# Kernel optimization log

Hardware: AMD Instinct MI355X
Metric: run time of the kernel (lower is better)

## Reference

```python
import jax, jax.numpy as jnp
import numpy as np
from jax import lax


def setup_inputs() -> dict:
    key = jax.random.key(0)
    k1, k2 = jax.random.split(key)
    x = jax.random.normal(k1, (32, 128, 64, 64), dtype=jnp.float32)
    # learned kernel, original shape (k, k, in_channels, out_channels)
    K = jax.random.normal(k2, (3, 3, 128, 256), dtype=jnp.float32) * 0.05
    return {"x": x, "K": K}


def reference(x, K):
    stride, padding = 1, 1
    kh = K.shape[0]
    C = K.shape[2]
    O = K.shape[3]
    H = x.shape[-1]
    P = H + 2 * padding
    out_size = (P - kh) // stride + 1
    # Original pairs x-patches flattened as (C, kh, kw) with K flattened
    # row-major as (kh, kw, C), matched purely by flat index. Equivalent to a
    # standard conv with the weight buffer reinterpreted as (C, kh, kw, O):
    W = K.reshape(-1, O).reshape(C, kh, kh, O).transpose(3, 0, 1, 2)  # (O,C,kh,kw)
    out = lax.conv_general_dilated(
        x, W,
        window_strides=(stride, stride),
        padding=[(padding, padding), (padding, padding)],
        dimension_numbers=("NCHW", "OIHW", "NCHW"),
    )  # (B, O, out_size, out_size)
    # Original loop uses range(0, P - kh, stride) (missing +1): when
    # (P - kh) % stride == 0 the last output row/col is never written (stays 0).
    n_filled = -(-(P - kh) // stride)  # ceil((P-kh)/stride), static
    if n_filled < out_size:
        out = out.at[:, :, n_filled:, :].set(0.0)
        out = out.at[:, :, :, n_filled:].set(0.0)
    return out
```

## Files before the change

### kernel.cpp

```cpp
#include <hip/hip_runtime.h>
#include <hip/hip_bf16.h>

typedef __attribute__((ext_vector_type(8))) short bf16x8;
typedef __attribute__((ext_vector_type(4))) float f32x4;

#define CIN   128
#define HW    64
#define OUTC  256

#define BP_OFF     33554432ULL
#define ZP_OFF     34144256ULL
#define WS_NEEDED  34148352ULL

#define SB  __builtin_amdgcn_s_barrier()
#define SCB __builtin_amdgcn_sched_barrier(0)
#define WAITV(N) asm volatile("s_waitcnt vmcnt(" #N ")" ::: "memory")
#define WAITL    asm volatile("s_waitcnt lgkmcnt(0)" ::: "memory")
#define MFMA(a, b, c) __builtin_amdgcn_mfma_f32_16x16x32_bf16(a, b, c, 0, 0, 0)

#define MFMA16(MB, A0, A1, A2, A3, B0, B1, B2, B3) do {            \
    __builtin_amdgcn_s_setprio(1);                                 \
    acc[MB+0][0] = MFMA(A0, B0, acc[MB+0][0]);                     \
    acc[MB+1][0] = MFMA(A1, B0, acc[MB+1][0]);                     \
    acc[MB+2][0] = MFMA(A2, B0, acc[MB+2][0]);                     \
    acc[MB+3][0] = MFMA(A3, B0, acc[MB+3][0]);                     \
    acc[MB+0][1] = MFMA(A0, B1, acc[MB+0][1]);                     \
    acc[MB+1][1] = MFMA(A1, B1, acc[MB+1][1]);                     \
    acc[MB+2][1] = MFMA(A2, B1, acc[MB+2][1]);                     \
    acc[MB+3][1] = MFMA(A3, B1, acc[MB+3][1]);                     \
    acc[MB+0][2] = MFMA(A0, B2, acc[MB+0][2]);                     \
    acc[MB+1][2] = MFMA(A1, B2, acc[MB+1][2]);                     \
    acc[MB+2][2] = MFMA(A2, B2, acc[MB+2][2]);                     \
    acc[MB+3][2] = MFMA(A3, B2, acc[MB+3][2]);                     \
    acc[MB+0][3] = MFMA(A0, B3, acc[MB+0][3]);                     \
    acc[MB+1][3] = MFMA(A1, B3, acc[MB+1][3]);                     \
    acc[MB+2][3] = MFMA(A2, B3, acc[MB+2][3]);                     \
    acc[MB+3][3] = MFMA(A3, B3, acc[MB+3][3]);                     \
    __builtin_amdgcn_s_setprio(0);                                 \
} while (0)

__global__ __launch_bounds__(256) void conv_prep(const float* __restrict__ X,
                                                 const float* __restrict__ Kw,
                                                 __hip_bfloat16* __restrict__ Xt,
                                                 __hip_bfloat16* __restrict__ Bp,
                                                 __hip_bfloat16* __restrict__ zp) {
    const int blk = blockIdx.x;
    if (blk < 2048) {
        __shared__ __hip_bfloat16 L[64][136];
        const int b = blk >> 6;
        const int y = blk & 63;
        const int x = threadIdx.x & 63;
        const int c0 = (threadIdx.x >> 6) * 32;
        const float* src = X + (((long)(b * CIN + c0) * HW + y) * HW + x);
        #pragma unroll
        for (int j = 0; j < 32; j += 2) {
            float v0 = src[(long)j * (HW * HW)];
            float v1 = src[(long)(j + 1) * (HW * HW)];
            __hip_bfloat162 p;
            p.x = __float2bfloat16(v0);
            p.y = __float2bfloat16(v1);
            *reinterpret_cast<__hip_bfloat162*>(&L[x][c0 + j]) = p;
        }
        __syncthreads();
        __hip_bfloat16* dst = Xt + (long)blk * (64 * 128);
        #pragma unroll
        for (int it = 0; it < 4; ++it) {
            int G = it * 256 + threadIdx.x;
            int xx = G >> 4, g = G & 15;
            bf16x8 v = *reinterpret_cast<const bf16x8*>(&L[xx][g * 8]);
            *reinterpret_cast<bf16x8*>(&dst[(long)G * 8]) = v;
        }
    } else if (blk < 2112) {
        for (int idx = (blk - 2048) * 256 + threadIdx.x; idx < 294912; idx += 64 * 256) {
            int c  = idx & 127;
            int n  = (idx >> 7) & 255;
            int ij = idx >> 15;
            Bp[idx] = __float2bfloat16(Kw[((c * 9 + ij) << 8) + n]);
        }
    } else {
        *reinterpret_cast<float4*>((char*)zp + threadIdx.x * 16) = float4{0.f, 0.f, 0.f, 0.f};
    }
}

__global__ __launch_bounds__(512, 2) void conv_igemm5(
    const __hip_bfloat16* __restrict__ Xt,
    const __hip_bfloat16* __restrict__ Bp,
    const __hip_bfloat16* __restrict__ zp,
    float* __restrict__ out)
{
    __shared__ __hip_bfloat16 As[2][2][256 * 32];
    __shared__ __hip_bfloat16 Bs[2][2][256 * 32];

    const int tid  = threadIdx.x;
    const int wv   = tid >> 6;
    const int lane = tid & 63;
    const int l16  = lane & 15;
    const int d16  = lane >> 4;
    const int wr   = wv >> 2;
    const int wc   = wv & 3;

    const int bid   = blockIdx.x;
    const int mtile = (bid & 7) * 64 + (bid >> 3);
    const int b  = mtile >> 4;
    const int y0 = (mtile & 15) * 4;

    const int srow = lane >> 2;
    const int sg   = lane & 3;

    f32x4 acc[8][4] = {};

    const int r0  = wv * 32 + srow;
    const int r1  = r0 + 16;
    const int G0  = (sg - (r0 >> 1)) & 3;
    const int G1  = (sg - (r1 >> 1)) & 3;
    const int xr0 = r0 & 63, xr1 = r1 & 63;
    const int yy0 = y0 + (r0 >> 6), yy1 = y0 + (r1 >> 6);
    const __hip_bfloat16* pA0 = Xt + (((long)b * 4096 + yy0 * 64 + xr0) * 128 + G0 * 8);
    const __hip_bfloat16* pA1 = Xt + (((long)b * 4096 + yy1 * 64 + xr1) * 128 + G1 * 8);
    const __hip_bfloat16* pB0 = Bp + ((long)r0 * 128 + G0 * 8);
    const __hip_bfloat16* pB1 = Bp + ((long)r1 * 128 + G1 * 8);
    const int ldsOff0 = (wv * 32) * 32;
    const int ldsOff1 = (wv * 32 + 16) * 32;

    auto stageA = [&](int t, int kh) {
        const int ij = t >> 1;
        const int c0 = (t & 1) * 64 + kh * 32;
        const int di = ij / 3 - 1;
        const int dj = ij % 3 - 1;
        const long off = (long)(di * 64 + dj) * 128 + c0;
        const bool ok0 = ((unsigned)(xr0 + dj) < 64u) && ((unsigned)(yy0 + di) < 64u);
        const bool ok1 = ((unsigned)(xr1 + dj) < 64u) && ((unsigned)(yy1 + di) < 64u);
        const __hip_bfloat16* g0 = ok0 ? pA0 + off : zp + c0;
        const __hip_bfloat16* g1 = ok1 ? pA1 + off : zp + c0;
        __builtin_amdgcn_global_load_lds(
            (const __attribute__((address_space(1))) void*)g0,
            (__attribute__((address_space(3))) void*)(&As[t & 1][kh][0] + ldsOff0), 16, 0, 0);
        __builtin_amdgcn_global_load_lds(
            (const __attribute__((address_space(1))) void*)g1,
            (__attribute__((address_space(3))) void*)(&As[t & 1][kh][0] + ldsOff1), 16, 0, 0);
    };
    auto stageB = [&](int t, int kh) {
        const long off = (long)(t >> 1) * 32768 + (t & 1) * 64 + kh * 32;
        __builtin_amdgcn_global_load_lds(
            (const __attribute__((address_space(1))) void*)(pB0 + off),
            (__attribute__((address_space(3))) void*)(&Bs[t & 1][kh][0] + ldsOff0), 16, 0, 0);
        __builtin_amdgcn_global_load_lds(
            (const __attribute__((address_space(1))) void*)(pB1 + off),
            (__attribute__((address_space(3))) void*)(&Bs[t & 1][kh][0] + ldsOff1), 16, 0, 0);
    };
    auto rdA = [&](int d, int kh, int mi) -> bf16x8 {
        const int m = wr * 128 + mi * 16 + l16;
        const int s = (d16 + (m >> 1)) & 3;
        return *reinterpret_cast<const bf16x8*>(&As[d][kh][m * 32 + s * 8]);
    };
    auto rdB = [&](int d, int kh, int ni) -> bf16x8 {
        const int n = wc * 64 + ni * 16 + l16;
        const int s = (d16 + (n >> 1)) & 3;
        return *reinterpret_cast<const bf16x8*>(&Bs[d][kh][n * 32 + s * 8]);
    };

    stageA(0, 0); stageB(0, 0);
    stageA(0, 1); stageB(0, 1);
    stageA(1, 0); stageB(1, 0);

    #define PAIR(D, KH, VW, STA, STB)                                        \
    do {                                                                     \
        STA;                                                                 \
        VW; SB; SCB;                                                         \
        bf16x8 A0 = rdA(D, KH, 0), A1 = rdA(D, KH, 1),                       \
               A2 = rdA(D, KH, 2), A3 = rdA(D, KH, 3);                       \
        bf16x8 B0 = rdB(D, KH, 0), B1 = rdB(D, KH, 1),                       \
               B2 = rdB(D, KH, 2), B3 = rdB(D, KH, 3);                       \
        WAITL; SCB;                                                          \
        MFMA16(0, A0, A1, A2, A3, B0, B1, B2, B3);                           \
        SB;                                                                  \
        STB;                                                                 \
        bf16x8 A4 = rdA(D, KH, 4), A5 = rdA(D, KH, 5),                       \
               A6 = rdA(D, KH, 6), A7 = rdA(D, KH, 7);                       \
        SB; WAITL; SCB;                                                      \
        MFMA16(4, A4, A5, A6, A7, B0, B1, B2, B3);                           \
        SB;                                                                  \
    } while (0)

    #pragma unroll
    for (int i = 0; i < 8; ++i) {
        const int t = 2 * i;
        PAIR(0, 0, WAITV(10), stageA(t + 1, 1), stageB(t + 1, 1));
        PAIR(0, 1, WAITV(10), stageA(t + 2, 0), stageB(t + 2, 0));
        PAIR(1, 0, WAITV(10), stageA(t + 2, 1), stageB(t + 2, 1));
        PAIR(1, 1, WAITV(10), stageA(t + 3, 0), stageB(t + 3, 0));
    }
    PAIR(0, 0, WAITV(10), stageA(17, 1), stageB(17, 1));
    PAIR(0, 1, WAITV(8),  (void)0, (void)0);
    PAIR(1, 0, WAITV(4),  (void)0, (void)0);
    PAIR(1, 1, WAITV(0),  (void)0, (void)0);
    #undef PAIR

    #pragma unroll
    for (int mi = 0; mi < 8; ++mi) {
        const int m  = wr * 128 + mi * 16 + d16 * 4;
        const int x0 = m & 63;
        const int y  = y0 + (m >> 6);
        #pragma unroll
        for (int ni = 0; ni < 4; ++ni) {
            const int o = wc * 64 + ni * 16 + l16;
            float4 v;
            v.x = acc[mi][ni][0];
            v.y = acc[mi][ni][1];
            v.z = acc[mi][ni][2];
            v.w = acc[mi][ni][3];
            if (y == HW - 1) { v.x = v.y = v.z = v.w = 0.f; }
            if (x0 + 3 == HW - 1) v.w = 0.f;
            *reinterpret_cast<float4*>(
                out + ((long)(b * OUTC + o) * 4096 + y * 64 + x0)) = v;
        }
    }
}

__global__ __launch_bounds__(256) void conv_igemm_bf16(
    const float* __restrict__ X, const float* __restrict__ Kw, float* __restrict__ out) {
    __shared__ __hip_bfloat16 As[128][40];
    __shared__ __hip_bfloat16 Bs[128][40];
    const int tid = threadIdx.x, wave = tid >> 6, lane = tid & 63;
    const int l16 = lane & 15, d16 = lane >> 4;
    const int m_base = blockIdx.x * 128;
    const int b = m_base >> 12, y0 = (m_base & 4095) >> 6;
    const int n_base = blockIdx.y * 128;
    const int wm = (wave >> 1) * 64, wn = (wave & 1) * 64;
    f32x4 acc[4][4] = {};
    const int smm = tid & 127, ccb = tid >> 7;
    const int sx = smm & 63, syr = smm >> 6;
    for (int ij = 0; ij < 9; ++ij) {
        const int di = ij / 3 - 1, dj = ij % 3 - 1;
        const int xp = sx + dj, yp = y0 + syr + di;
        const bool ok = ((unsigned)xp < 64u) && ((unsigned)yp < 64u);
        const long xbase = (((long)b * CIN) * HW + yp) * HW + xp;
        for (int c0 = 0; c0 < CIN; c0 += 32) {
            for (int cc = ccb; cc < 32; cc += 2) {
                float v = ok ? X[xbase + (long)(c0 + cc) * 4096] : 0.f;
                As[smm][cc] = __float2bfloat16(v);
                Bs[smm][cc] = __float2bfloat16(Kw[((c0 + cc) * 9 + ij) * OUTC + n_base + smm]);
            }
            __syncthreads();
            bf16x8 afrag[4], bfrag[4];
            for (int mi = 0; mi < 4; ++mi)
                afrag[mi] = *reinterpret_cast<const bf16x8*>(&As[wm + mi * 16 + l16][d16 * 8]);
            for (int ni = 0; ni < 4; ++ni)
                bfrag[ni] = *reinterpret_cast<const bf16x8*>(&Bs[wn + ni * 16 + l16][d16 * 8]);
            for (int mi = 0; mi < 4; ++mi)
                for (int ni = 0; ni < 4; ++ni)
                    acc[mi][ni] = __builtin_amdgcn_mfma_f32_16x16x32_bf16(
                        afrag[mi], bfrag[ni], acc[mi][ni], 0, 0, 0);
            __syncthreads();
        }
    }
    for (int mi = 0; mi < 4; ++mi)
        for (int ni = 0; ni < 4; ++ni)
            for (int r = 0; r < 4; ++r) {
                const int mm = wm + mi * 16 + d16 * 4 + r;
                const int nn = wn + ni * 16 + l16;
                const int y = y0 + (mm >> 6), x = mm & 63, o = n_base + nn;
                float v = acc[mi][ni][r];
                if (y == 63 || x == 63) v = 0.f;
                out[(((long)b * OUTC + o) * HW + y) * HW + x] = v;
            }
}

extern "C" void kernel_launch(void* const* d_in, const int* in_sizes, int n_in,
                              void* d_out, int out_size, void* d_ws, size_t ws_size,
                              hipStream_t stream) {
    const float* X  = (const float*)d_in[0];
    const float* Kw = (const float*)d_in[1];
    float* out = (float*)d_out;

    if (ws_size >= WS_NEEDED) {
        char* ws = (char*)d_ws;
        __hip_bfloat16* Xt = (__hip_bfloat16*)ws;
        __hip_bfloat16* Bp = (__hip_bfloat16*)(ws + BP_OFF);
        __hip_bfloat16* zp = (__hip_bfloat16*)(ws + ZP_OFF);
        conv_prep<<<dim3(2113), dim3(256), 0, stream>>>(X, Kw, Xt, Bp, zp);
        conv_igemm5<<<dim3(512), dim3(512), 0, stream>>>(Xt, Bp, zp, out);
    } else {
        conv_igemm_bf16<<<dim3(1024, 2), dim3(256), 0, stream>>>(X, Kw, out);
    }
}
```

Measured before the change: 107.4 us.

## Restructure conv main loop into 4-stage LDS ring with one barrier pair per k-step

Replaces the hand-interleaved double-buffer PAIR schedule, which split each 32-wide k-slice into two half-MFMA batches with mid-step staging, with a uniform 4-deep ring buffer of 32-channel slices. Each of the 36 iterations reads all A/B fragments into registers, issues the global-to-LDS load for slice H+3, waits on vmcnt, then runs all 32 MFMAs under raised priority. This simplifies the schedule and keeps three slices in flight. In exchange it holds 12 fragment vectors live at once, which raises register pressure, and the compiler has less fine-grained interleaving of LDS reads with MFMAs.

```diff
diff --git a/kernel.cpp b/kernel.cpp
--- a/kernel.cpp
+++ b/kernel.cpp
@@ -15,29 +15,7 @@
 #define SB  __builtin_amdgcn_s_barrier()
 #define SCB __builtin_amdgcn_sched_barrier(0)
 #define WAITV(N) asm volatile("s_waitcnt vmcnt(" #N ")" ::: "memory")
-#define WAITL    asm volatile("s_waitcnt lgkmcnt(0)" ::: "memory")
 #define MFMA(a, b, c) __builtin_amdgcn_mfma_f32_16x16x32_bf16(a, b, c, 0, 0, 0)
-
-#define MFMA16(MB, A0, A1, A2, A3, B0, B1, B2, B3) do {            \
-    __builtin_amdgcn_s_setprio(1);                                 \
-    acc[MB+0][0] = MFMA(A0, B0, acc[MB+0][0]);                     \
-    acc[MB+1][0] = MFMA(A1, B0, acc[MB+1][0]);                     \
-    acc[MB+2][0] = MFMA(A2, B0, acc[MB+2][0]);                     \
-    acc[MB+3][0] = MFMA(A3, B0, acc[MB+3][0]);                     \
-    acc[MB+0][1] = MFMA(A0, B1, acc[MB+0][1]);                     \
-    acc[MB+1][1] = MFMA(A1, B1, acc[MB+1][1]);                     \
-    acc[MB+2][1] = MFMA(A2, B1, acc[MB+2][1]);                     \
-    acc[MB+3][1] = MFMA(A3, B1, acc[MB+3][1]);                     \
-    acc[MB+0][2] = MFMA(A0, B2, acc[MB+0][2]);                     \
-    acc[MB+1][2] = MFMA(A1, B2, acc[MB+1][2]);                     \
-    acc[MB+2][2] = MFMA(A2, B2, acc[MB+2][2]);                     \
-    acc[MB+3][2] = MFMA(A3, B2, acc[MB+3][2]);                     \
-    acc[MB+0][3] = MFMA(A0, B3, acc[MB+0][3]);                     \
-    acc[MB+1][3] = MFMA(A1, B3, acc[MB+1][3]);                     \
-    acc[MB+2][3] = MFMA(A2, B3, acc[MB+2][3]);                     \
-    acc[MB+3][3] = MFMA(A3, B3, acc[MB+3][3]);                     \
-    __builtin_amdgcn_s_setprio(0);                                 \
-} while (0)
 
 __global__ __launch_bounds__(256) void conv_prep(const float* __restrict__ X,
                                                  const float* __restrict__ Kw,
@@ -82,14 +60,14 @@
     }
 }
 
-__global__ __launch_bounds__(512, 2) void conv_igemm5(
+__global__ __launch_bounds__(512, 2) void conv_igemm6(
     const __hip_bfloat16* __restrict__ Xt,
     const __hip_bfloat16* __restrict__ Bp,
     const __hip_bfloat16* __restrict__ zp,
     float* __restrict__ out)
 {
-    __shared__ __hip_bfloat16 As[2][2][256 * 32];
-    __shared__ __hip_bfloat16 Bs[2][2][256 * 32];
+    __shared__ __hip_bfloat16 As[4][256 * 32];
+    __shared__ __hip_bfloat16 Bs[4][256 * 32];
 
     const int tid  = threadIdx.x;
     const int wv   = tid >> 6;
@@ -122,79 +100,67 @@
     const int ldsOff0 = (wv * 32) * 32;
     const int ldsOff1 = (wv * 32 + 16) * 32;
 
-    auto stageA = [&](int t, int kh) {
-        const int ij = t >> 1;
-        const int c0 = (t & 1) * 64 + kh * 32;
+    auto stage = [&](int S) {
+        const int ij = S >> 2;
+        const int c0 = (S & 3) * 32;
         const int di = ij / 3 - 1;
         const int dj = ij % 3 - 1;
-        const long off = (long)(di * 64 + dj) * 128 + c0;
+        const long offA = (long)(di * 64 + dj) * 128 + c0;
         const bool ok0 = ((unsigned)(xr0 + dj) < 64u) && ((unsigned)(yy0 + di) < 64u);
         const bool ok1 = ((unsigned)(xr1 + dj) < 64u) && ((unsigned)(yy1 + di) < 64u);
-        const __hip_bfloat16* g0 = ok0 ? pA0 + off : zp + c0;
-        const __hip_bfloat16* g1 = ok1 ? pA1 + off : zp + c0;
-        __builtin_amdgcn_global_load_lds(
-            (const __attribute__((address_space(1))) void*)g0,
-            (__attribute__((address_space(3))) void*)(&As[t & 1][kh][0] + ldsOff0), 16, 0, 0);
-        __builtin_amdgcn_global_load_lds(
-            (const __attribute__((address_space(1))) void*)g1,
-            (__attribute__((address_space(3))) void*)(&As[t & 1][kh][0] + ldsOff1), 16, 0, 0);
+        const __hip_bfloat16* gA0 = ok0 ? pA0 + offA : zp + c0;
+        const __hip_bfloat16* gA1 = ok1 ? pA1 + offA : zp + c0;
+        __hip_bfloat16* ldsA = &As[S & 3][0];
+        __builtin_amdgcn_global_load_lds(
+            (const __attribute__((address_space(1))) void*)gA0,
+            (__attribute__((address_space(3))) void*)(ldsA + ldsOff0), 16, 0, 0);
+        __builtin_amdgcn_global_load_lds(
+            (const __attribute__((address_space(1))) void*)gA1,
+            (__attribute__((address_space(3))) void*)(ldsA + ldsOff1), 16, 0, 0);
+        const long offB = (long)ij * 32768 + c0;
+        __hip_bfloat16* ldsB = &Bs[S & 3][0];
+        __builtin_amdgcn_global_load_lds(
+            (const __attribute__((address_space(1))) void*)(pB0 + offB),
+            (__attribute__((address_space(3))) void*)(ldsB + ldsOff0), 16, 0, 0);
+        __builtin_amdgcn_global_load_lds(
+            (const __attribute__((address_space(1))) void*)(pB1 + offB),
+            (__attribute__((address_space(3))) void*)(ldsB + ldsOff1), 16, 0, 0);
     };
-    auto stageB = [&](int t, int kh) {
-        const long off = (long)(t >> 1) * 32768 + (t & 1) * 64 + kh * 32;
-        __builtin_amdgcn_global_load_lds(
-            (const __attribute__((address_space(1))) void*)(pB0 + off),
-            (__attribute__((address_space(3))) void*)(&Bs[t & 1][kh][0] + ldsOff0), 16, 0, 0);
-        __builtin_amdgcn_global_load_lds(
-            (const __attribute__((address_space(1))) void*)(pB1 + off),
-            (__attribute__((address_space(3))) void*)(&Bs[t & 1][kh][0] + ldsOff1), 16, 0, 0);
-    };
-    auto rdA = [&](int d, int kh, int mi) -> bf16x8 {
-        const int m = wr * 128 + mi * 16 + l16;
-        const int s = (d16 + (m >> 1)) & 3;
-        return *reinterpret_cast<const bf16x8*>(&As[d][kh][m * 32 + s * 8]);
-    };
-    auto rdB = [&](int d, int kh, int ni) -> bf16x8 {
-        const int n = wc * 64 + ni * 16 + l16;
-        const int s = (d16 + (n >> 1)) & 3;
-        return *reinterpret_cast<const bf16x8*>(&Bs[d][kh][n * 32 + s * 8]);
-    };
-
-    stageA(0, 0); stageB(0, 0);
-    stageA(0, 1); stageB(0, 1);
-    stageA(1, 0); stageB(1, 0);
-
-    #define PAIR(D, KH, VW, STA, STB)                                        \
-    do {                                                                     \
-        STA;                                                                 \
-        VW; SB; SCB;                                                         \
-        bf16x8 A0 = rdA(D, KH, 0), A1 = rdA(D, KH, 1),                       \
-               A2 = rdA(D, KH, 2), A3 = rdA(D, KH, 3);                       \
-        bf16x8 B0 = rdB(D, KH, 0), B1 = rdB(D, KH, 1),                       \
-               B2 = rdB(D, KH, 2), B3 = rdB(D, KH, 3);                       \
-        WAITL; SCB;                                                          \
-        MFMA16(0, A0, A1, A2, A3, B0, B1, B2, B3);                           \
-        SB;                                                                  \
-        STB;                                                                 \
-        bf16x8 A4 = rdA(D, KH, 4), A5 = rdA(D, KH, 5),                       \
-               A6 = rdA(D, KH, 6), A7 = rdA(D, KH, 7);                       \
-        SB; WAITL; SCB;                                                      \
-        MFMA16(4, A4, A5, A6, A7, B0, B1, B2, B3);                           \
-        SB;                                                                  \
-    } while (0)
+
+    stage(0); stage(1); stage(2);
+    WAITV(8);
+    SCB; SB;
 
     #pragma unroll
-    for (int i = 0; i < 8; ++i) {
-        const int t = 2 * i;
-        PAIR(0, 0, WAITV(10), stageA(t + 1, 1), stageB(t + 1, 1));
-        PAIR(0, 1, WAITV(10), stageA(t + 2, 0), stageB(t + 2, 0));
-        PAIR(1, 0, WAITV(10), stageA(t + 2, 1), stageB(t + 2, 1));
-        PAIR(1, 1, WAITV(10), stageA(t + 3, 0), stageB(t + 3, 0));
-    }
-    PAIR(0, 0, WAITV(10), stageA(17, 1), stageB(17, 1));
-    PAIR(0, 1, WAITV(8),  (void)0, (void)0);
-    PAIR(1, 0, WAITV(4),  (void)0, (void)0);
-    PAIR(1, 1, WAITV(0),  (void)0, (void)0);
-    #undef PAIR
+    for (int H = 0; H < 36; ++H) {
+        const int RB = H & 3;
+        bf16x8 Af[8], Bf[4];
+        #pragma unroll
+        for (int mi = 0; mi < 8; ++mi) {
+            const int m = wr * 128 + mi * 16 + l16;
+            const int s = (d16 + (m >> 1)) & 3;
+            Af[mi] = *reinterpret_cast<const bf16x8*>(&As[RB][m * 32 + s * 8]);
+        }
+        #pragma unroll
+        for (int ni = 0; ni < 4; ++ni) {
+            const int n = wc * 64 + ni * 16 + l16;
+            const int s = (d16 + (n >> 1)) & 3;
+            Bf[ni] = *reinterpret_cast<const bf16x8*>(&Bs[RB][n * 32 + s * 8]);
+        }
+        if (H < 33) stage(H + 3);
+        if (H < 33)       WAITV(8);
+        else if (H == 33) WAITV(4);
+        else if (H == 34) WAITV(0);
+        SCB; SB;
+        __builtin_amdgcn_s_setprio(1);
+        #pragma unroll
+        for (int ni = 0; ni < 4; ++ni)
+            #pragma unroll
+            for (int mi = 0; mi < 8; ++mi)
+                acc[mi][ni] = MFMA(Af[mi], Bf[ni], acc[mi][ni]);
+        __builtin_amdgcn_s_setprio(0);
+        SCB; SB;
+    }
 
     #pragma unroll
     for (int mi = 0; mi < 8; ++mi) {
@@ -279,7 +245,7 @@
         __hip_bfloat16* Bp = (__hip_bfloat16*)(ws + BP_OFF);
         __hip_bfloat16* zp = (__hip_bfloat16*)(ws + ZP_OFF);
         conv_prep<<<dim3(2113), dim3(256), 0, stream>>>(X, Kw, Xt, Bp, zp);
-        conv_igemm5<<<dim3(512), dim3(512), 0, stream>>>(Xt, Bp, zp, out);
+        conv_igemm6<<<dim3(512), dim3(512), 0, stream>>>(Xt, Bp, zp, out);
     } else {
         conv_igemm_bf16<<<dim3(1024, 2), dim3(256), 0, stream>>>(X, Kw, out);
     }
```

Result: no change. 109.1 us (+1.6%).
